# Kernel optimization log

Measured on AMD Instinct MI355X. Metric: run time of the kernel, lower is better.

The kernel has to match this reference:

```python
import jax, jax.numpy as jnp
import numpy as np

B, S, T, D = 16, 512, 16, 128
LN_EPS = 1e-5


def setup_inputs() -> dict:
    key = jax.random.key(0)
    k_x, k_h, k_w = jax.random.split(key, 3)
    x = jax.random.normal(k_x, (B, S, T, D), dtype=jnp.float32)
    # prev_hidden must be strictly positive (code takes its log)
    prev_hidden = jax.random.uniform(k_h, (B, 1, T, D), dtype=jnp.float32) * 0.9 + 0.05
    ln_gamma = jnp.ones((D,), jnp.float32)
    ln_beta = jnp.zeros((D,), jnp.float32)
    # torch Linear(dim, 2*dim): store as (D, 2D) for x @ W
    W = jax.random.normal(k_w, (D, 2 * D), dtype=jnp.float32) * (1.0 / np.sqrt(D))
    b = jnp.zeros((2 * D,), jnp.float32)
    return {"x": x, "prev_hidden": prev_hidden, "ln_gamma": ln_gamma,
            "ln_beta": ln_beta, "W": W, "b": b}


def _g_act_log(h):
    # log of G activation: x>=0 -> log(relu(x)+0.5); x<0 -> -softplus(-x)
    return jnp.where(h >= 0, jnp.log(jax.nn.relu(h) + 0.5), -jax.nn.softplus(-h))


def reference(x, prev_hidden, ln_gamma, ln_beta, W, b):
    seq_len = x.shape[1]
    # LayerNorm over last dim
    mu = jnp.mean(x, axis=-1, keepdims=True)
    var = jnp.var(x, axis=-1, keepdims=True)
    xn = (x - mu) * jax.lax.rsqrt(var + LN_EPS) * ln_gamma + ln_beta
    gh = jnp.einsum('bstd,de->bste', xn, W) + b  # (B,S,T,2D)
    gate, hidden = jnp.split(gh, 2, axis=-1)
    # parallel (seq_len > 1) log-space path
    log_coeffs = -jax.nn.softplus(gate)          # log(1 - z)
    log_z = -jax.nn.softplus(-gate)              # log z
    log_values = log_z + _g_act_log(hidden)      # (B,S,T,D)
    # prepend prev_hidden: values get log(h0), coeffs get zero pad
    log_values = jnp.concatenate([jnp.log(prev_hidden), log_values], axis=1)
    zero_pad = jnp.zeros_like(log_coeffs[:, :1])
    log_coeffs = jnp.concatenate([zero_pad, log_coeffs], axis=1)
    # Heinsen associative scan in log space
    a_star = jnp.cumsum(log_coeffs, axis=1)
    log_h0_plus_b_star = jax.lax.cumlogsumexp(log_values - a_star, axis=1)
    out = jnp.exp(a_star + log_h0_plus_b_star)
    out = out[:, -seq_len:]
    next_prev_hidden = out[:, -1:]
    return out, next_prev_hidden
```

## Files before the change

kernel.cpp:

```cpp
#include <hip/hip_runtime.h>
#include <hip/hip_bf16.h>
#include <stdint.h>

#define BB 16
#define SS 512
#define TT 16
#define DD 128
#define CH 64
#define NCH (SS/CH)
#define LN_EPS 1e-5f

typedef __attribute__((ext_vector_type(8))) short short8;
typedef __attribute__((ext_vector_type(4))) float f32x4;

static __device__ __forceinline__ uint32_t cvt_pk_bf16(float lo, float hi) {
    uint32_t r;
    asm("v_cvt_pk_bf16_f32 %0, %1, %2" : "=v"(r) : "v"(lo), "v"(hi));
    return r;
}

#define BAR() do {                                            \
    asm volatile("s_waitcnt lgkmcnt(0)" ::: "memory");        \
    __builtin_amdgcn_s_barrier();                             \
    asm volatile("" ::: "memory");                            \
} while (0)

__global__ __launch_bounds__(512, 2) void fused_mingru(
    const float* __restrict__ x, const float* __restrict__ prevh,
    const float* __restrict__ gamma, const float* __restrict__ beta,
    const float* __restrict__ W, const float* __restrict__ bias,
    float* __restrict__ out, float* __restrict__ nexth)
{
    __shared__ __align__(16) unsigned char xnb[2][CH*256];

    const int tid  = threadIdx.x;
    const int w    = tid >> 6;
    const int lane = tid & 63;
    const int l15  = lane & 15;
    const int lhi  = lane >> 4;

    const int bt = blockIdx.x;
    const size_t rowstride = (size_t)TT * DD;
    const size_t base_bt   = ((size_t)(bt >> 4) * SS * TT + (bt & 15)) * DD;

    const int r_ln = tid >> 3;
    const int c8   = tid & 7;
    const int slot_p = ((r_ln >> 2) & 3)*16 + (r_ln >> 4)*4 + (r_ln & 3);
    const int keyx   = slot_p & 7;
    const float* xp0 = x + base_bt + (size_t)r_ln * rowstride + c8*16;

    f32x4 px0, px1, px2, px3;
    auto issuePx = [&](int st) {
        const float* xp = xp0 + (size_t)st * CH * rowstride;
        px0 = *(const f32x4*)(xp + 0);
        px1 = *(const f32x4*)(xp + 4);
        px2 = *(const f32x4*)(xp + 8);
        px3 = *(const f32x4*)(xp + 12);
    };
    issuePx(0);

    short8 wfr[2][4];
    float  bs2[2];
    #pragma unroll
    for (int ni = 0; ni < 2; ++ni) {
        const int col = (ni ? 128 : 0) + w*16 + l15;
        float acc = 0.0f;
        #pragma unroll
        for (int kt = 0; kt < 4; ++kt) {
            union { short8 s8; uint32_t u[4]; } fr;
            #pragma unroll
            for (int p = 0; p < 4; ++p) {
                const int k0 = kt*32 + lhi*8 + 2*p;
                const float w0 = W[(size_t)k0*256 + col];
                const float w1 = W[(size_t)(k0+1)*256 + col];
                acc = fmaf(beta[k0],   w0, acc);
                acc = fmaf(beta[k0+1], w1, acc);
                fr.u[p] = cvt_pk_bf16(gamma[k0]*w0, gamma[k0+1]*w1);
            }
            wfr[ni][kt] = fr.s8;
        }
        acc += __shfl_xor(acc, 16);
        acc += __shfl_xor(acc, 32);
        bs2[ni] = bias[col] + acc;
    }

    float hM = prevh[(size_t)bt*128 + w*16 + l15];

    auto phaseLN = [&](int st) {
        float s1 = px0.x+px0.y+px0.z+px0.w + px1.x+px1.y+px1.z+px1.w
                 + px2.x+px2.y+px2.z+px2.w + px3.x+px3.y+px3.z+px3.w;
        float s2 = px0.x*px0.x+px0.y*px0.y+px0.z*px0.z+px0.w*px0.w
                 + px1.x*px1.x+px1.y*px1.y+px1.z*px1.z+px1.w*px1.w
                 + px2.x*px2.x+px2.y*px2.y+px2.z*px2.z+px2.w*px2.w
                 + px3.x*px3.x+px3.y*px3.y+px3.z*px3.z+px3.w*px3.w;
        s1 += __shfl_xor(s1, 1); s2 += __shfl_xor(s2, 1);
        s1 += __shfl_xor(s1, 2); s2 += __shfl_xor(s2, 2);
        s1 += __shfl_xor(s1, 4); s2 += __shfl_xor(s2, 4);
        const float mu = s1 * (1.0f/128.0f);
        const float rs = rsqrtf(s2 * (1.0f/128.0f) - mu*mu + LN_EPS);
        unsigned char* row = xnb[st & 1] + slot_p*256;
        union { short8 s8; uint32_t u[4]; } a, b2;
        a.u[0]  = cvt_pk_bf16((px0.x-mu)*rs, (px0.y-mu)*rs);
        a.u[1]  = cvt_pk_bf16((px0.z-mu)*rs, (px0.w-mu)*rs);
        a.u[2]  = cvt_pk_bf16((px1.x-mu)*rs, (px1.y-mu)*rs);
        a.u[3]  = cvt_pk_bf16((px1.z-mu)*rs, (px1.w-mu)*rs);
        b2.u[0] = cvt_pk_bf16((px2.x-mu)*rs, (px2.y-mu)*rs);
        b2.u[1] = cvt_pk_bf16((px2.z-mu)*rs, (px2.w-mu)*rs);
        b2.u[2] = cvt_pk_bf16((px3.x-mu)*rs, (px3.y-mu)*rs);
        b2.u[3] = cvt_pk_bf16((px3.z-mu)*rs, (px3.w-mu)*rs);
        *(short8*)(row + (((2*c8)     ^ keyx) << 4)) = a.s8;
        *(short8*)(row + (((2*c8 + 1) ^ keyx) << 4)) = b2.s8;
    };

    auto phaseG = [&](int st) {
        const unsigned char* xb = xnb[st & 1];
        float Cc[16], Cv[16];
        #pragma unroll
        for (int mt = 0; mt < 4; ++mt) {
            const unsigned char* rowp = xb + (mt*16 + l15)*256;
            short8 af[4];
            #pragma unroll
            for (int kt = 0; kt < 4; ++kt) {
                const int c = (kt << 2) | lhi;
                af[kt] = *(const short8*)(rowp + ((c ^ (l15 & 7)) << 4));
            }
            f32x4 ag = (f32x4)(0.f), ah = (f32x4)(0.f);
            #pragma unroll
            for (int kt = 0; kt < 4; ++kt) {
                ag = __builtin_amdgcn_mfma_f32_16x16x32_bf16(af[kt], wfr[0][kt], ag, 0, 0, 0);
                ah = __builtin_amdgcn_mfma_f32_16x16x32_bf16(af[kt], wfr[1][kt], ah, 0, 0, 0);
            }
            #pragma unroll
            for (int j = 0; j < 4; ++j) {
                const float g  = ag[j] + bs2[0];
                const float hh = ah[j] + bs2[1];
                const float cc = 1.0f / (1.0f + __expf(g));
                const float ga = (hh >= 0.0f) ? (hh + 0.5f)
                                              : (1.0f / (1.0f + __expf(-hh)));
                Cc[mt*4 + j] = cc;
                Cv[mt*4 + j] = (1.0f - cc) * ga;
            }
        }
        #pragma unroll
        for (int i = 1; i < 16; ++i) {
            Cv[i] = fmaf(Cc[i], Cv[i-1], Cv[i]);
            Cc[i] = Cc[i] * Cc[i-1];
        }
        float Ic = Cc[15], Iv = Cv[15];
        float pc = __shfl_up(Ic, 16), pv = __shfl_up(Iv, 16);
        if (lhi >= 1) { Iv = fmaf(Ic, pv, Iv); Ic *= pc; }
        pc = __shfl_up(Ic, 32); pv = __shfl_up(Iv, 32);
        if (lhi >= 2) { Iv = fmaf(Ic, pv, Iv); Ic *= pc; }
        float Ec = __shfl_up(Ic, 16), Ev = __shfl_up(Iv, 16);
        if (lhi == 0) { Ec = 1.0f; Ev = 0.0f; }
        const float Mc = __shfl(Ic, 48 + l15);
        const float Mv = __shfl(Iv, 48 + l15);
        const float hE = fmaf(Ec, hM, Ev);
        float* op = out + base_bt + (size_t)(st*CH + lhi*16) * rowstride + w*16 + l15;
        #pragma unroll
        for (int i = 0; i < 16; ++i)
            op[(size_t)i * rowstride] = fmaf(Cc[i], hE, Cv[i]);
        hM = fmaf(Mc, hM, Mv);
    };

    phaseLN(0);
    issuePx(1);
    BAR();

    for (int st = 0; st < NCH; ++st) {
        phaseG(st);
        if (st + 1 < NCH) {
            phaseLN(st + 1);
            if (st + 2 < NCH) issuePx(st + 2);
        }
        BAR();
    }

    if (lane < 16)
        nexth[(size_t)bt*128 + w*16 + lane] = hM;
}

extern "C" void kernel_launch(void* const* d_in, const int* in_sizes, int n_in,
                              void* d_out, int out_size, void* d_ws, size_t ws_size,
                              hipStream_t stream) {
    const float* x     = (const float*)d_in[0];
    const float* prevh = (const float*)d_in[1];
    const float* gamma = (const float*)d_in[2];
    const float* beta  = (const float*)d_in[3];
    const float* W     = (const float*)d_in[4];
    const float* bias  = (const float*)d_in[5];

    float* out   = (float*)d_out;
    float* nexth = out + (size_t)BB*SS*TT*DD;

    fused_mingru<<<BB*TT, 512, 0, stream>>>(x, prevh, gamma, beta, W, bias,
                                            out, nexth);
}
```

Measured before the change: 41.93 us.

## Split scan into two-pass chunked kernels to parallelize across sequence chunks

Replaces the single kernel, where each block walks all 8 sequence chunks serially, with two launches of 8x more blocks, one per (batch,time,chunk). Pass 1 computes per-chunk scan carries (coefficient, value) into workspace. Pass 2 recomputes LayerNorm, GEMM and the local scan, folds the prefix carries from earlier chunks, and writes outputs. This targets the low block count (256 blocks on a 256-CU GPU) and the serial chunk dependency, at the cost of reading x twice, redoing the GEMM and activations, and an extra launch.

```diff
diff --git a/kernel.cpp b/kernel.cpp
--- a/kernel.cpp
+++ b/kernel.cpp
@@ -25,13 +25,16 @@
     asm volatile("" ::: "memory");                            \
 } while (0)
 
-__global__ __launch_bounds__(512, 2) void fused_mingru(
+template<int PASS>
+__global__ __launch_bounds__(512, 4)
+void mingru_pass(
     const float* __restrict__ x, const float* __restrict__ prevh,
     const float* __restrict__ gamma, const float* __restrict__ beta,
     const float* __restrict__ W, const float* __restrict__ bias,
-    float* __restrict__ out, float* __restrict__ nexth)
+    float2* __restrict__ cws, float* __restrict__ out,
+    float* __restrict__ nexth)
 {
-    __shared__ __align__(16) unsigned char xnb[2][CH*256];
+    __shared__ __align__(16) unsigned char xnb[CH*256];
 
     const int tid  = threadIdx.x;
     const int w    = tid >> 6;
@@ -39,7 +42,9 @@
     const int l15  = lane & 15;
     const int lhi  = lane >> 4;
 
-    const int bt = blockIdx.x;
+    const int bid = blockIdx.x;
+    const int bt  = bid >> 3;
+    const int ch  = bid & 7;
     const size_t rowstride = (size_t)TT * DD;
     const size_t base_bt   = ((size_t)(bt >> 4) * SS * TT + (bt & 15)) * DD;
 
@@ -47,17 +52,12 @@
     const int c8   = tid & 7;
     const int slot_p = ((r_ln >> 2) & 3)*16 + (r_ln >> 4)*4 + (r_ln & 3);
     const int keyx   = slot_p & 7;
-    const float* xp0 = x + base_bt + (size_t)r_ln * rowstride + c8*16;
 
-    f32x4 px0, px1, px2, px3;
-    auto issuePx = [&](int st) {
-        const float* xp = xp0 + (size_t)st * CH * rowstride;
-        px0 = *(const f32x4*)(xp + 0);
-        px1 = *(const f32x4*)(xp + 4);
-        px2 = *(const f32x4*)(xp + 8);
-        px3 = *(const f32x4*)(xp + 12);
-    };
-    issuePx(0);
+    const float* xp = x + base_bt + (size_t)(ch*CH + r_ln)*rowstride + c8*16;
+    const f32x4 px0 = *(const f32x4*)(xp + 0);
+    const f32x4 px1 = *(const f32x4*)(xp + 4);
+    const f32x4 px2 = *(const f32x4*)(xp + 8);
+    const f32x4 px3 = *(const f32x4*)(xp + 12);
 
     short8 wfr[2][4];
     float  bs2[2];
@@ -84,9 +84,7 @@
         bs2[ni] = bias[col] + acc;
     }
 
-    float hM = prevh[(size_t)bt*128 + w*16 + l15];
-
-    auto phaseLN = [&](int st) {
+    {
         float s1 = px0.x+px0.y+px0.z+px0.w + px1.x+px1.y+px1.z+px1.w
                  + px2.x+px2.y+px2.z+px2.w + px3.x+px3.y+px3.z+px3.w;
         float s2 = px0.x*px0.x+px0.y*px0.y+px0.z*px0.z+px0.w*px0.w
@@ -98,7 +96,7 @@
         s1 += __shfl_xor(s1, 4); s2 += __shfl_xor(s2, 4);
         const float mu = s1 * (1.0f/128.0f);
         const float rs = rsqrtf(s2 * (1.0f/128.0f) - mu*mu + LN_EPS);
-        unsigned char* row = xnb[st & 1] + slot_p*256;
+        unsigned char* row = xnb + slot_p*256;
         union { short8 s8; uint32_t u[4]; } a, b2;
         a.u[0]  = cvt_pk_bf16((px0.x-mu)*rs, (px0.y-mu)*rs);
         a.u[1]  = cvt_pk_bf16((px0.z-mu)*rs, (px0.w-mu)*rs);
@@ -110,74 +108,68 @@
         b2.u[3] = cvt_pk_bf16((px3.z-mu)*rs, (px3.w-mu)*rs);
         *(short8*)(row + (((2*c8)     ^ keyx) << 4)) = a.s8;
         *(short8*)(row + (((2*c8 + 1) ^ keyx) << 4)) = b2.s8;
-    };
+    }
+    BAR();
 
-    auto phaseG = [&](int st) {
-        const unsigned char* xb = xnb[st & 1];
-        float Cc[16], Cv[16];
+    float Cc[16], Cv[16];
+    #pragma unroll
+    for (int mt = 0; mt < 4; ++mt) {
+        const unsigned char* rowp = xnb + (mt*16 + l15)*256;
+        short8 af[4];
         #pragma unroll
-        for (int mt = 0; mt < 4; ++mt) {
-            const unsigned char* rowp = xb + (mt*16 + l15)*256;
-            short8 af[4];
-            #pragma unroll
-            for (int kt = 0; kt < 4; ++kt) {
-                const int c = (kt << 2) | lhi;
-                af[kt] = *(const short8*)(rowp + ((c ^ (l15 & 7)) << 4));
-            }
-            f32x4 ag = (f32x4)(0.f), ah = (f32x4)(0.f);
-            #pragma unroll
-            for (int kt = 0; kt < 4; ++kt) {
-                ag = __builtin_amdgcn_mfma_f32_16x16x32_bf16(af[kt], wfr[0][kt], ag, 0, 0, 0);
-                ah = __builtin_amdgcn_mfma_f32_16x16x32_bf16(af[kt], wfr[1][kt], ah, 0, 0, 0);
-            }
-            #pragma unroll
-            for (int j = 0; j < 4; ++j) {
-                const float g  = ag[j] + bs2[0];
-                const float hh = ah[j] + bs2[1];
-                const float cc = 1.0f / (1.0f + __expf(g));
-                const float ga = (hh >= 0.0f) ? (hh + 0.5f)
-                                              : (1.0f / (1.0f + __expf(-hh)));
-                Cc[mt*4 + j] = cc;
-                Cv[mt*4 + j] = (1.0f - cc) * ga;
-            }
+        for (int kt = 0; kt < 4; ++kt) {
+            const int c = (kt << 2) | lhi;
+            af[kt] = *(const short8*)(rowp + ((c ^ (l15 & 7)) << 4));
+        }
+        f32x4 ag = (f32x4)(0.f), ah = (f32x4)(0.f);
+        #pragma unroll
+        for (int kt = 0; kt < 4; ++kt) {
+            ag = __builtin_amdgcn_mfma_f32_16x16x32_bf16(af[kt], wfr[0][kt], ag, 0, 0, 0);
+            ah = __builtin_amdgcn_mfma_f32_16x16x32_bf16(af[kt], wfr[1][kt], ah, 0, 0, 0);
         }
         #pragma unroll
-        for (int i = 1; i < 16; ++i) {
-            Cv[i] = fmaf(Cc[i], Cv[i-1], Cv[i]);
-            Cc[i] = Cc[i] * Cc[i-1];
+        for (int j = 0; j < 4; ++j) {
+            const float g  = ag[j] + bs2[0];
+            const float hh = ah[j] + bs2[1];
+            const float cc = 1.0f / (1.0f + __expf(g));
+            const float ga = (hh >= 0.0f) ? (hh + 0.5f)
+                                          : (1.0f / (1.0f + __expf(-hh)));
+            Cc[mt*4 + j] = cc;
+            Cv[mt*4 + j] = (1.0f - cc) * ga;
         }
-        float Ic = Cc[15], Iv = Cv[15];
-        float pc = __shfl_up(Ic, 16), pv = __shfl_up(Iv, 16);
-        if (lhi >= 1) { Iv = fmaf(Ic, pv, Iv); Ic *= pc; }
-        pc = __shfl_up(Ic, 32); pv = __shfl_up(Iv, 32);
-        if (lhi >= 2) { Iv = fmaf(Ic, pv, Iv); Ic *= pc; }
+    }
+    #pragma unroll
+    for (int i = 1; i < 16; ++i) {
+        Cv[i] = fmaf(Cc[i], Cv[i-1], Cv[i]);
+        Cc[i] = Cc[i] * Cc[i-1];
+    }
+    float Ic = Cc[15], Iv = Cv[15];
+    float pc = __shfl_up(Ic, 16), pv = __shfl_up(Iv, 16);
+    if (lhi >= 1) { Iv = fmaf(Ic, pv, Iv); Ic *= pc; }
+    pc = __shfl_up(Ic, 32); pv = __shfl_up(Iv, 32);
+    if (lhi >= 2) { Iv = fmaf(Ic, pv, Iv); Ic *= pc; }
+    const float Mc = __shfl(Ic, 48 + l15);
+    const float Mv = __shfl(Iv, 48 + l15);
+
+    if constexpr (PASS == 1) {
+        if (lane < 16)
+            cws[(size_t)bid*128 + w*16 + lane] = make_float2(Mc, Mv);
+    } else {
         float Ec = __shfl_up(Ic, 16), Ev = __shfl_up(Iv, 16);
         if (lhi == 0) { Ec = 1.0f; Ev = 0.0f; }
-        const float Mc = __shfl(Ic, 48 + l15);
-        const float Mv = __shfl(Iv, 48 + l15);
-        const float hE = fmaf(Ec, hM, Ev);
-        float* op = out + base_bt + (size_t)(st*CH + lhi*16) * rowstride + w*16 + l15;
+        float h = prevh[(size_t)bt*128 + w*16 + l15];
+        for (int k = 0; k < ch; ++k) {
+            const float2 m = cws[((size_t)bt*8 + k)*128 + w*16 + l15];
+            h = fmaf(m.x, h, m.y);
+        }
+        const float hE = fmaf(Ec, h, Ev);
+        float* op = out + base_bt + (size_t)(ch*CH + lhi*16) * rowstride + w*16 + l15;
         #pragma unroll
         for (int i = 0; i < 16; ++i)
             op[(size_t)i * rowstride] = fmaf(Cc[i], hE, Cv[i]);
-        hM = fmaf(Mc, hM, Mv);
-    };
-
-    phaseLN(0);
-    issuePx(1);
-    BAR();
-
-    for (int st = 0; st < NCH; ++st) {
-        phaseG(st);
-        if (st + 1 < NCH) {
-            phaseLN(st + 1);
-            if (st + 2 < NCH) issuePx(st + 2);
-        }
-        BAR();
+        if (ch == 7 && lane < 16)
+            nexth[(size_t)bt*128 + w*16 + lane] = fmaf(Mc, h, Mv);
     }
-
-    if (lane < 16)
-        nexth[(size_t)bt*128 + w*16 + lane] = hM;
 }
 
 extern "C" void kernel_launch(void* const* d_in, const int* in_sizes, int n_in,
@@ -192,7 +184,10 @@
 
     float* out   = (float*)d_out;
     float* nexth = out + (size_t)BB*SS*TT*DD;
+    float2* cws  = (float2*)d_ws;
 
-    fused_mingru<<<BB*TT, 512, 0, stream>>>(x, prevh, gamma, beta, W, bias,
-                                            out, nexth);
+    mingru_pass<1><<<BB*TT*NCH, 512, 0, stream>>>(x, prevh, gamma, beta, W,
+                                                  bias, cws, out, nexth);
+    mingru_pass<2><<<BB*TT*NCH, 512, 0, stream>>>(x, prevh, gamma, beta, W,
+                                                  bias, cws, out, nexth);
 }
```

New measurement: 92.33 us. +120.2%, slower.
